# Kernel optimization log

Measured on AMD Instinct MI355X. Metric: run time of the kernel, lower is better.

Reference implementation:

```python
import jax, jax.numpy as jnp
import numpy as np

B, C, H, W = 16, 256, 56, 56
HID = C * 2            # modifier_expansion = 2
GROUPS = 8             # min(8, HID//4)
K = 3                  # inner_steps
LR = 0.01              # exp(log(inner_lr))
RATIO = 0.25           # spatial_mask_ratio
GN_EPS = 1e-5


def setup_inputs() -> dict:
    key = jax.random.key(0)
    ks = jax.random.split(key, 12)
    x = jax.random.normal(ks[0], (B, C, H, W), jnp.float32)
    # modifier params (1x1 convs stored as 2D matrices) + GroupNorm affine
    conv1_w = jax.random.normal(ks[1], (HID, C), jnp.float32) / np.sqrt(C)
    gn_gamma = 1.0 + 0.1 * jax.random.normal(ks[2], (HID,), jnp.float32)
    gn_beta = 0.1 * jax.random.normal(ks[3], (HID,), jnp.float32)
    conv2_w = jax.random.normal(ks[4], (C, HID), jnp.float32) / np.sqrt(HID)
    # surprise reconstructor (bottleneck = C//4)
    recon_w1 = jax.random.normal(ks[5], (C // 4, C), jnp.float32) / np.sqrt(C)
    recon_w2 = jax.random.normal(ks[6], (C, C // 4), jnp.float32) / np.sqrt(C // 4)
    # gate MLP
    gate_w1 = jax.random.normal(ks[7], (C // 4, C), jnp.float32) / np.sqrt(C)
    gate_b1 = jnp.zeros((C // 4,), jnp.float32)
    gate_w2 = jax.random.normal(ks[8], (1, C // 4), jnp.float32) / np.sqrt(C // 4)
    gate_b2 = jnp.zeros((1,), jnp.float32)
    residual_scale = jnp.asarray(0.05, jnp.float32)
    # EMA buffers (eval mode: frozen)
    running_mean = 0.05 * jax.random.normal(ks[9], (C,), jnp.float32)
    running_var = 1.0 + 0.05 * jax.random.uniform(ks[10], (C,), jnp.float32)
    # spatial masks: exactly int(H*W*RATIO) zeroed positions per sample, one mask
    # per inner update step (only steps 0..K-2 affect the output)
    num_mask = int(H * W * RATIO)
    rng = np.random.default_rng(0)
    r = rng.random((K - 1, B, H * W))
    idx = np.argsort(r, axis=-1)[..., :num_mask]
    m = np.ones((K - 1, B, H * W), dtype=bool)
    np.put_along_axis(m, idx, False, axis=-1)
    masks = jnp.asarray(m.reshape(K - 1, B, 1, H, W))
    return dict(x=x, conv1_w=conv1_w, gn_gamma=gn_gamma, gn_beta=gn_beta,
                conv2_w=conv2_w, recon_w1=recon_w1, recon_w2=recon_w2,
                gate_w1=gate_w1, gate_b1=gate_b1, gate_w2=gate_w2,
                gate_b2=gate_b2, residual_scale=residual_scale,
                running_mean=running_mean, running_var=running_var, masks=masks)


def _group_norm(h, gamma, beta):
    b = h.shape[0]
    hg = h.reshape(b, GROUPS, HID // GROUPS, H, W)
    mu = hg.mean(axis=(2, 3, 4), keepdims=True)
    var = hg.var(axis=(2, 3, 4), keepdims=True)  # biased, matching torch GN
    hg = (hg - mu) * jax.lax.rsqrt(var + GN_EPS)
    return hg.reshape(b, HID, H, W) * gamma[None, :, None, None] + beta[None, :, None, None]


def _modifier(feat, w1, gamma, beta, w2):
    # Conv2d 1x1 (no bias) -> GroupNorm -> GELU -> [Dropout2d: identity in eval] -> Conv2d 1x1
    h = jnp.einsum('bchw,oc->bohw', feat, w1)
    h = jax.nn.gelu(_group_norm(h, gamma, beta), approximate=False)
    return jnp.einsum('bohw,co->bchw', h, w2)


def _surprise(y, mask, rw1, rw2, rm, rv):
    mf = mask.astype(y.dtype)                       # [B,1,H,W]
    my = y * mf
    h = jax.nn.gelu(jnp.einsum('bchw,oc->bohw', my, rw1), approximate=False)
    rec = jnp.einsum('bohw,co->bchw', h, rw2)
    inv = 1.0 - mf
    recon = (((rec - y) ** 2) * inv).sum() / (inv.sum() * C + 1e-8)
    n = y.shape[0] * y.shape[2] * y.shape[3]
    cm = y.mean(axis=(0, 2, 3))                     # [C]
    cv = ((y - cm[None, :, None, None]) ** 2).sum(axis=(0, 2, 3)) / (n - 1)  # unbiased
    consist = ((cm - rm) ** 2).mean() + ((cv / (rv + 1e-8) - 1.0) ** 2).mean()
    return recon + 0.1 * consist


def reference(x, conv1_w, gn_gamma, gn_beta, conv2_w, recon_w1, recon_w2,
              gate_w1, gate_b1, gate_w2, gate_b2, residual_scale,
              running_mean, running_var, masks):
    feat = jax.lax.stop_gradient(x)  # feat_inner = features.detach()
    params = (conv1_w, gn_gamma, gn_beta, conv2_w)

    def inner_loss(p, mask):
        m = _modifier(feat, *p)
        return _surprise(m + feat, mask, recon_w1, recon_w2, running_mean, running_var)

    # TTT inner loop: K-1 SGD updates on the modifier params; updates are
    # stop_gradient'ed so the outer Jacobian wrt initial params is identity,
    # matching torch's .data in-place update with create_graph=False.
    for step in range(K - 1):
        g = jax.grad(inner_loss)(params, masks[step])
        params = tuple(p - LR * jax.lax.stop_gradient(gi) for p, gi in zip(params, g))

    modification = _modifier(x, *params)  # final forward uses non-detached features

    pooled = x.mean(axis=(2, 3))                                    # [B,C]
    gh = jax.nn.gelu(pooled @ gate_w1.T + gate_b1, approximate=False)
    gate = jax.nn.sigmoid(gh @ gate_w2.T + gate_b2)[:, :, None, None]  # [B,1,1,1]

    return x + residual_scale * gate * modification
```

## Files before the change

### kernel.cpp

```cpp
#include <hip/hip_runtime.h>
#include <math.h>


#define BB    16
#define CC    256
#define HWW   3136
#define NTOT  (BB*HWW)
#define HIDD  512
#define NGRP  8
#define GMSZ  (64*HWW)
#define C4    64
#define LRATE 0.01f
#define SKW   32
#define CHUNK (NTOT/SKW)
#define NV8   (HWW/8)
#define FSTR  132

#define EP_STORE    0
#define EP_ADDFEAT  1
#define EP_T1H      2
#define EP_DYREC    3
#define EP_DT1      4
#define EP_DYFIN    5
#define EP_H1STAT   6
// ... 90 lines not shown

__global__ void k_cvt(const void* __restrict__ src, float* __restrict__ dst, int n,
                      const int* __restrict__ dtf){
  int i = blockIdx.x*256 + threadIdx.x;
  if (i>=n) return;
  if (*dtf) dst[i] = bf2f(((const u16*)src)[i]);
  else      dst[i] = ((const float*)src)[i];
}
__global__ void k_wcvt(const float* __restrict__ src, u16* __restrict__ d,
                       u16* __restrict__ dT, int R, int Cc){
  int i = blockIdx.x*256+threadIdx.x;
  if (i >= R*Cc) return;
  int r = i/Cc, c = i - r*Cc;
  u16 v = f2bf(src[i]);
  d[i] = v;
  if (dT) dT[(size_t)c*R + r] = v;
}

__global__ void k_expand(const unsigned char* __restrict__ mraw, const int* __restrict__ flag,
                         float* __restrict__ mf, float* __restrict__ zc){
  __shared__ float sm[4];
  int i = blockIdx.x*256 + threadIdx.x;
  int f = *flag;
  float v;
  if (f==1)      v = (((const int*)mraw)[i] != 0) ? 1.f : 0.f;
  else if (f==0) v = (mraw[i] != 0) ? 1.f : 0.f;
  else if (f==2) v = (((const u16*)mraw)[i] != 0) ? 1.f : 0.f;
  else           v = (((const float*)mraw)[i] != 0.f) ? 1.f : 0.f;
  mf[i] = v;
  float S = blk_sum(1.f - v, sm);
  if (threadIdx.x==0) atomicAdd(&zc[blockIdx.x/196], S);
}

template<int MASKX,int EPI,int XDYN,int E0DYN>
__global__ __launch_bounds__(256) void k_gemm_mfma(
    const u16* __restrict__ A, const void* __restrict__ Xv, u16* __restrict__ Out,
    int K, const int* __restrict__ xdt, const float* __restrict__ mf,
    const void* __restrict__ e0, const float* __restrict__ e1,
    const float* __restrict__ e2, u16* __restrict__ o2, float* __restrict__ o3)
{
  __shared__ __align__(16) u16 Ws[64*40];
  __shared__ __align__(16) u16 Xs[128*40];
  const int t = threadIdx.x;
  const int w = t >> 6, lane = t & 63;
  const int col = lane & 15, quad = lane >> 4;
  const int M = (int)gridDim.y << 6;
  const int m0 = blockIdx.y << 6, n0 = blockIdx.x << 7;
  const int isbx = XDYN ? *xdt : 1;
  const u16*   Xb = (const u16*)Xv;
  const float* Xf = (const float*)Xv;
  const int wrow = t >> 2, wkq = (t & 3) * 8;
  const int xn   = 2*(t & 63);
  const int xq   = t >> 6;
  const int gn0  = n0 + xn;
  const int xb_  = gn0 / HWW;
  const int xs_  = gn0 - xb_*HWW;

  f32x4 acc[4][2];
  #pragma unroll
  for (int i=0;i<4;i++){
    #pragma unroll
    for (int j=0;j<2;j++) acc[i][j] = (f32x4)(0.0f);
  }

  for (int k0=0; k0<K; k0+=32){
    {
      uint4 v = *(const uint4*)(A + (size_t)(m0+wrow)*K + k0 + wkq);
      *(uint4*)(Ws + wrow*40 + wkq) = v;
    }
    {
      ushort e[16];
      size_t base = ((size_t)xb_*K + k0 + xq*8)*HWW + xs_;
      if (isbx){
        #pragma unroll
        for (int j=0;j<8;j++){
          unsigned v = *(const unsigned*)(Xb + base + (size_t)j*HWW);
          e[j]   = (ushort)(v & 0xFFFFu);
          e[8+j] = (ushort)(v >> 16);
        }
      } else {
        #pragma unroll
        for (int j=0;j<8;j++){
          float2 f = *(const float2*)(Xf + base + (size_t)j*HWW);
          e[j]   = f2bf(f.x);
          e[8+j] = f2bf(f.y);
        }
      }
      if (MASKX){
        if (mf[gn0]   == 0.f){
          #pragma unroll
          for (int j=0;j<8;j++) e[j] = 0;
        }
        if (mf[gn0+1] == 0.f){
          #pragma unroll
          for (int j=0;j<8;j++) e[8+j] = 0;
        }
      }
      *(uint4*)(Xs + xn*40     + xq*8) = pack8(e);
      *(uint4*)(Xs + (xn+1)*40 + xq*8) = pack8(e+8);
    }
    __syncthreads();
    bf16x8 af[4], bfr[2];
    #pragma unroll
    for (int mi=0;mi<4;mi++)
      af[mi] = *(const bf16x8*)(Ws + (mi*16+col)*40 + quad*8);
    #pragma unroll
    for (int nj=0;nj<2;nj++)
      bfr[nj] = *(const bf16x8*)(Xs + (w*32+nj*16+col)*40 + quad*8);
    #pragma unroll
    for (int mi=0;mi<4;mi++){
      #pragma unroll
      for (int nj=0;nj<2;nj++)
        acc[mi][nj] = __builtin_amdgcn_mfma_f32_16x16x32_bf16(af[mi], bfr[nj], acc[mi][nj], 0,0,0);
    }
    __syncthreads();
  }
  const int isb0 = E0DYN ? *xdt : 1;
  float* fst  = (float*)Xs;
  float* sred = (float*)Ws;
  const int row16 = t >> 4;
  const int cb    = (t & 15) * 8;
  const int nb8   = n0 + cb;
  const int b8    = nb8 / HWW;
  const int sb8   = nb8 - b8*HWW;
  const int bA    = n0 / HWW, bB = (n0+127)/HWW;
  const int g     = m0 >> 6;

  if (EPI==EP_H1STAT){ if (t<4) sred[t]=0.f; }
  if (EPI==EP_YADDSTAT){ for (int i=t;i<128;i+=256) sred[i]=0.f; }
  if (EPI==EP_GNB1){ for (int i=t;i<132;i+=256) sred[i]=0.f; }
  if (EPI==EP_H1STAT||EPI==EP_YADDSTAT||EPI==EP_GNB1) __syncthreads();

  float dscale=0.f, gmul=0.f, muT=0.f, rT=0.f;
  if (EPI==EP_DYREC) dscale = 2.0f / (e1[0]*(float)CC + 1e-8f);
  if (EPI==EP_OUT)   gmul = e2[0]*e1[b8];
  if (EPI==EP_GNB1){ muT = e1[b8*NGRP+g]; rT = e1[128+b8*NGRP+g]; }

  #pragma unroll
  for (int mi=0;mi<4;mi++){
    #pragma unroll
    for (int nj=0;nj<2;nj++){
      #pragma unroll
      for (int r=0;r<4;r++)
        fst[(quad*4+r)*FSTR + w*32 + nj*16 + col] = acc[mi][nj][r];
    }
    __syncthreads();
    const int m = m0 + mi*16 + row16;
    const size_t oidx = ((size_t)b8*M + m)*HWW + sb8;
    float v[8];
    {
      const float* frow = fst + row16*FSTR + cb;
      float4 p0 = *(const float4*)frow;
      float4 p1 = *(const float4*)(frow+4);
      v[0]=p0.x; v[1]=p0.y; v[2]=p0.z; v[3]=p0.w;
      v[4]=p1.x; v[5]=p1.y; v[6]=p1.z; v[7]=p1.w;
    }

    if (EPI==EP_STORE){
      *(uint4*)(Out+oidx) = pk8(v);
    }
    else if (EPI==EP_ADDFEAT){
      float xv[8];
      if (isb0) up8(*(const uint4*)((const u16*)e0+oidx), xv);
      else {
        float4 a0 = *(const float4*)((const float*)e0+oidx);
        float4 a1 = *(const float4*)((const float*)e0+oidx+4);
        xv[0]=a0.x; xv[1]=a0.y; xv[2]=a0.z; xv[3]=a0.w;
        xv[4]=a1.x; xv[5]=a1.y; xv[6]=a1.z; xv[7]=a1.w;
      }
      #pragma unroll
      for (int j=0;j<8;j++) v[j] += xv[j];
      *(uint4*)(Out+oidx) = pk8(v);
// ... 11 lines not shown
      float4 f0 = *(const float4*)(mf+nb8);
      float4 f1 = *(const float4*)(mf+nb8+4);
      mfv[0]=f0.x; mfv[1]=f0.y; mfv[2]=f0.z; mfv[3]=f0.w;
      mfv[4]=f1.x; mfv[5]=f1.y; mfv[6]=f1.z; mfv[7]=f1.w;
      #pragma unroll
      for (int j=0;j<8;j++) v[j] = (v[j]-yv[j])*(1.0f-mfv[j])*dscale;
      *(uint4*)(Out+oidx) = pk8(v);
    }
    else if (EPI==EP_DT1){
      float tv[8];
      up8(*(const uint4*)((const u16*)e0+oidx), tv);
      #pragma unroll
      for (int j=0;j<8;j++) v[j] = v[j]*gelu_g_fast(tv[j]);
      *(uint4*)(Out+oidx) = pk8(v);
    }
    else if (EPI==EP_DYFIN){
      float yv[8], dv[8], mfv[8];
      up8(*(const uint4*)((const u16*)e0+oidx), yv);
      up8(*(const uint4*)(Out+oidx), dv);
      float4 f0 = *(const float4*)(mf+nb8);
      float4 f1 = *(const float4*)(mf+nb8+4);
      mfv[0]=f0.x; mfv[1]=f0.y; mfv[2]=f0.z; mfv[3]=f0.w;
      mfv[4]=f1.x; mfv[5]=f1.y; mfv[6]=f1.z; mfv[7]=f1.w;
      const float c1 = e1[m], c2 = e2[m];
      #pragma unroll
      for (int j=0;j<8;j++) v[j] = mfv[j]*v[j] - dv[j] + c1 + c2*yv[j];
      *(uint4*)(Out+oidx) = pk8(v);
    }
    else if (EPI==EP_H1STAT){
      *(uint4*)(Out+oidx) = pk8(v);
      float s=0.f, q=0.f;
      #pragma unroll
      for (int j=0;j<8;j++){ s += v[j]; q = fmaf(v[j],v[j],q); }
      float s0 = (b8==bA)?s:0.f, q0 = (b8==bA)?q:0.f;
      float s1v = s-s0, q1v = q-q0;
      #pragma unroll
      for (int o=1;o<64;o<<=1){
        s0 += __shfl_xor(s0,o); q0 += __shfl_xor(q0,o);
        s1v += __shfl_xor(s1v,o); q1v += __shfl_xor(q1v,o);
      }
      if (lane==0){
        atomicAdd(&sred[0], s0); atomicAdd(&sred[1], q0);
        atomicAdd(&sred[2], s1v); atomicAdd(&sred[3], q1v);
      }
    }
    else if (EPI==EP_YADDSTAT){
      float xv[8];
      if (isb0) up8(*(const uint4*)((const u16*)e0+oidx), xv);
      else {
        float4 a0 = *(const float4*)((const float*)e0+oidx);
        float4 a1 = *(const float4*)((const float*)e0+oidx+4);
        xv[0]=a0.x; xv[1]=a0.y; xv[2]=a0.z; xv[3]=a0.w;
        xv[4]=a1.x; xv[5]=a1.y; xv[6]=a1.z; xv[7]=a1.w;
      }
      float s=0.f, q=0.f;
      #pragma unroll
      for (int j=0;j<8;j++){
        v[j] += xv[j];
        s += v[j]; q = fmaf(v[j],v[j],q);
      }
      *(uint4*)(Out+oidx) = pk8(v);
      #pragma unroll
      for (int o=1;o<16;o<<=1){ s += __shfl_xor(s,o); q += __shfl_xor(q,o); }
      if ((t&15)==0){
        atomicAdd(&sred[mi*16+row16], s);
        atomicAdd(&sred[64+mi*16+row16], q);
      }
    }
    else if (EPI==EP_GNB1){
      float hv[8];
      up8(*(const uint4*)((const u16*)e0+oidx), hv);
      const float go = e2[m], beo = e2[HIDD+m];
      float dB=0.f, dG=0.f, sS=0.f, sQ=0.f;
      #pragma unroll
      for (int j=0;j<8;j++){
        float hn   = (hv[j]-muT)*rT;
        float ghat = fmaf(hn, go, beo);
        float dgh  = v[j]*gelu_g_fast(ghat);
        float dhn  = dgh*go;
        v[j] = dhn;
        dB += dgh; dG = fmaf(dgh,hn,dG);
        sS += dhn; sQ = fmaf(dhn,hn,sQ);
      }
      *(uint4*)(Out+oidx) = pk8(v);
      #pragma unroll
      for (int o=1;o<16;o<<=1){ dB += __shfl_xor(dB,o); dG += __shfl_xor(dG,o); }
      if ((t&15)==0){
        atomicAdd(&sred[mi*16+row16], dB);
        atomicAdd(&sred[64+mi*16+row16], dG);
      }
      float s0 = (b8==bA)?sS:0.f, q0 = (b8==bA)?sQ:0.f;
      float s1v = sS-s0, q1v = sQ-q0;
      #pragma unroll
      for (int o=1;o<64;o<<=1){
        s0 += __shfl_xor(s0,o); q0 += __shfl_xor(q0,o);
        s1v += __shfl_xor(s1v,o); q1v += __shfl_xor(q1v,o);
      }
      if (lane==0){
        atomicAdd(&sred[128], s0); atomicAdd(&sred[129], q0);
        atomicAdd(&sred[130], s1v); atomicAdd(&sred[131], q1v);
      }
    }
    else if (EPI==EP_OUT){
      float xv[8];
      if (isb0){
        up8(*(const uint4*)((const u16*)e0+oidx), xv);
        #pragma unroll
        for (int j=0;j<8;j++) v[j] = xv[j] + gmul*v[j];
        *(uint4*)(Out+oidx) = pk8(v);
      } else {
        float4 a0 = *(const float4*)((const float*)e0+oidx);
        float4 a1 = *(const float4*)((const float*)e0+oidx+4);
        float4 r0, r1;
        r0.x = a0.x + gmul*v[0]; r0.y = a0.y + gmul*v[1];
        r0.z = a0.z + gmul*v[2]; r0.w = a0.w + gmul*v[3];
        r1.x = a1.x + gmul*v[4]; r1.y = a1.y + gmul*v[5];
        r1.z = a1.z + gmul*v[6]; r1.w = a1.w + gmul*v[7];
        *(float4*)((float*)Out+oidx)   = r0;
        *(float4*)((float*)Out+oidx+4) = r1;
      }
    }
    __syncthreads();
  }

  if (EPI==EP_H1STAT){
    if (t==0){
      atomicAdd(&o3[bA*NGRP+g],     sred[0]);
      atomicAdd(&o3[128+bA*NGRP+g], sred[1]);
    }
    if (t==1 && bB!=bA){
      atomicAdd(&o3[bB*NGRP+g],     sred[2]);
      atomicAdd(&o3[128+bB*NGRP+g], sred[3]);
    }
  }
  if (EPI==EP_YADDSTAT){
    if (t<64){
      atomicAdd(&o3[m0+t],    sred[t]);
      atomicAdd(&o3[CC+m0+t], sred[64+t]);
    }
  }
  if (EPI==EP_GNB1){
    if (t<64){
      atomicAdd(&o3[m0+t],     sred[64+t]);
      atomicAdd(&o3[512+m0+t], sred[t]);
    }
    if (t==64){
      atomicAdd(&o3[1024+bA*NGRP+g], sred[128]);
      atomicAdd(&o3[1152+bA*NGRP+g], sred[129]);
    }
    if (t==65 && bB!=bA){
      atomicAdd(&o3[1024+bB*NGRP+g], sred[130]);
      atomicAdd(&o3[1152+bB*NGRP+g], sred[131]);
    }
  }
}

template<int QDYN, int GNB2>
__global__ __launch_bounds__(256) void k_wgrad_mfma(
    const u16* __restrict__ P, const void* __restrict__ Qv, float* __restrict__ part,
    int CHP, int CHQ, const int* __restrict__ xdt, int ntx,
    const u16* __restrict__ h1, const float* __restrict__ musig,
    const float* __restrict__ red)
{
  __shared__ u16 Ps[64*40];
  __shared__ u16 Qs[64*40];
  const int f = blockIdx.x;
  const int j = f >> 3;
  const int sk = (f & 7) + ((j >> 5) << 3);
  const int tile = j & 31;
  const int ty = tile / ntx;
  const int m0 = (tile - ty*ntx) << 6;
  const int n0 = ty << 6;
  const int t = threadIdx.x;
  const int w = t >> 6, lane = t & 63;
  const int col = lane & 15, quad = lane >> 4;
  const int isbq = QDYN ? *xdt : 1;
  const u16*   Qb = (const u16*)Qv;
  const float* Qf = (const float*)Qv;
  const int srow = (t & 127) >> 1;
  const int ssq  = ((t & 127) & 1) * 16;
  f32x4 acc[2][2];
  #pragma unroll
  for (int i=0;i<2;i++){
    #pragma unroll
    for (int jj=0;jj<2;jj++) acc[i][jj] = (f32x4)(0.0f);
  }
  const int mbase = (w & 1)*32, nbase = (w >> 1)*32;

  for (int kb = sk*CHUNK; kb < sk*CHUNK + CHUNK; kb += 32){
    const int b = kb / HWW;
    const int s = kb - b*HWW;
    if (t < 128){
      size_t off = ((size_t)b*CHP + m0+srow)*HWW + s + ssq;
      uint4 v0 = *(const uint4*)(P + off);
      uint4 v1 = *(const uint4*)(P + off + 8);
      if (GNB2){
        const int bg = b*NGRP + (m0>>6);
        const float mu_ = musig[bg], r_ = musig[128+bg];
        const float a1 = red[1024+bg]*(1.0f/GMSZ);
        const float a2 = red[1152+bg]*(1.0f/GMSZ);
        uint4 h0 = *(const uint4*)(h1 + off);
        uint4 h1v = *(const uint4*)(h1 + off + 8);
        float fd[8], fh[8];
        up8(v0, fd); up8(h0, fh);
        #pragma unroll
        for (int q2=0;q2<8;q2++){ float hn=(fh[q2]-mu_)*r_; fd[q2]=r_*(fd[q2]-a1-hn*a2); }
        v0 = pk8(fd);
        up8(v1, fd); up8(h1v, fh);
        #pragma unroll
        for (int q2=0;q2<8;q2++){ float hn=(fh[q2]-mu_)*r_; fd[q2]=r_*(fd[q2]-a1-hn*a2); }
        v1 = pk8(fd);
      }
      *(uint4*)(Ps + srow*40 + ssq)     = v0;
      *(uint4*)(Ps + srow*40 + ssq + 8) = v1;
    } else {
      size_t off = ((size_t)b*CHQ + n0+srow)*HWW + s + ssq;
      if (isbq){
        uint4 v0 = *(const uint4*)(Qb + off);
        uint4 v1 = *(const uint4*)(Qb + off + 8);
        *(uint4*)(Qs + srow*40 + ssq)     = v0;
        *(uint4*)(Qs + srow*40 + ssq + 8) = v1;
      } else {
        ushort e[16];
        #pragma unroll
        for (int g2=0; g2<4; g2++){
          float4 ff = *(const float4*)(Qf + off + g2*4);
          e[g2*4+0]=f2bf(ff.x); e[g2*4+1]=f2bf(ff.y); e[g2*4+2]=f2bf(ff.z); e[g2*4+3]=f2bf(ff.w);
        }
        *(uint4*)(Qs + srow*40 + ssq)     = pack8(e);
        *(uint4*)(Qs + srow*40 + ssq + 8) = pack8(e+8);
      }
    }
    __syncthreads();
    bf16x8 pa[2], qb[2];
    #pragma unroll
    for (int a=0;a<2;a++)
      pa[a] = *(const bf16x8*)(Ps + (mbase + a*16 + col)*40 + quad*8);
    #pragma unroll
    for (int bb=0;bb<2;bb++)
      qb[bb] = *(const bf16x8*)(Qs + (nbase + bb*16 + col)*40 + quad*8);
    #pragma unroll
    for (int a=0;a<2;a++){
      #pragma unroll
      for (int bb=0;bb<2;bb++)
        acc[a][bb] = __builtin_amdgcn_mfma_f32_16x16x32_bf16(pa[a], qb[bb], acc[a][bb], 0,0,0);
    }
    __syncthreads();
  }
  float* dst = part + (size_t)sk*CHP*CHQ;
  #pragma unroll
  for (int a=0;a<2;a++){
    #pragma unroll
    for (int bb=0;bb<2;bb++){
      #pragma unroll
      for (int r=0;r<4;r++){
        const int m = m0 + mbase + a*16 + quad*4 + r;
        const int n = n0 + nbase + bb*16 + col;
        dst[(size_t)m*CHQ + n] = acc[a][bb][r];
      }
    }
  }
}
__global__ void k_wgrad_reduce(const float* __restrict__ part, float* __restrict__ dW, int n){
  int i = blockIdx.x*256+threadIdx.x;
  if (i>=n) return;
  float s=0;
  #pragma unroll
  for (int k=0;k<SKW;k++) s += part[(size_t)k*n + i];
  dW[i]=s;
}

__global__ void k_gn_finalize(const float* gsum, const float* gsumsq, float* mu, float* rsig){
  int i = threadIdx.x; if (i>=BB*NGRP) return;
// ... 204 lines not shown
  }
  u16* h1p = nullptr;
  if (off + (size_t)HIDD*NTOT*2 <= ws_size)
    h1p = (u16*)alloc((size_t)HIDD*NTOT*2);

  k_detect_dtype<<<1,1,0,stream>>>((const u16*)x_in, dtf);
  k_detect_mask<<<1,1,0,stream>>>((const unsigned char*)mk_in, mkf);
  #define CVT(src,dst,n) k_cvt<<<((n)+255)/256,256,0,stream>>>(src,dst,(n),dtf)
  CVT(w1_in,  pw1,  131072);
  CVT(g_in,   pg,   512);
  CVT(b_in,   pb,   512);
  CVT(w2_in,  pw2,  131072);
  CVT(rw1_in, rw1f, 16384);
  CVT(rw2_in, rw2f, 16384);
  CVT(gw1_in, gw1f, 16384);
  CVT(gb1_in, gb1f, 64);
  CVT(gw2_in, gw2f, 64);
  CVT(gb2_in, gb2f, 1);
  CVT(rs_in,  rsf,  1);
  CVT(rm_in,  rmf,  256);
  CVT(rv_in,  rvf,  256);
  #undef CVT
  k_wcvt<<<512,256,0,stream>>>(pw1, wb1, 0,     HIDD, CC);
  k_wcvt<<<512,256,0,stream>>>(pw2, wb2, wb2T,  CC, HIDD);
  k_wcvt<<<64,256,0,stream>>>(rw1f, rwb1, rwb1T, C4, CC);
  k_wcvt<<<64,256,0,stream>>>(rw2f, rwb2, rwb2T, CC, C4);
  hipMemsetAsync(zc, 0, 8, stream);
  k_expand<<<392,256,0,stream>>>((const unsigned char*)mk_in, mkf, mfb, zc);

  for (int s=0; s<2; s++){
    const float* mfs = mfb + s*NTOT;
    u16* h1dst = h1p ? h1p : Ab;
    hipMemsetAsync(gsum, 0, 1024, stream);
    k_gemm_mfma<0,EP_H1STAT,1,0><<<dim3(392,8),256,0,stream>>>(wb1, x_in, h1dst, CC, dtf, 0,0,0,0,0, gsum);
    k_gn_finalize<<<1,128,0,stream>>>(gsum, gsumsq, mu, rsig);
    k_gelu_fwd<1><<<BB*HIDD,256,0,stream>>>(h1dst, Ab, mu, rsig, pg, pb);
    hipMemsetAsync(cmsum, 0, 2048, stream);
    k_gemm_mfma<0,EP_YADDSTAT,0,1><<<dim3(392,4),256,0,stream>>>(wb2, Ab, ybuf, HIDD, dtf, 0, x_in, 0,0,0, cmsum);
    k_y_finalize<<<1,256,0,stream>>>(cmsum, cmsq, rmf, rvf, coefA, coefB);
    k_gemm_mfma<1,EP_T1H,0,0><<<dim3(392,1),256,0,stream>>>(rwb1, ybuf, t1b, CC, dtf, mfs, 0,0,0, hb, 0);
    k_gemm_mfma<0,EP_DYREC,0,0><<<dim3(392,4),256,0,stream>>>(rwb2, hb, dY, C4, dtf, mfs, ybuf, zc+s, 0,0, 0);
    k_gemm_mfma<0,EP_DT1,0,0><<<dim3(392,1),256,0,stream>>>(rwb2T, dY, hb, CC, dtf, 0, t1b, 0,0,0, 0);
    k_gemm_mfma<0,EP_DYFIN,0,0><<<dim3(392,4),256,0,stream>>>(rwb1T, hb, dY, C4, dtf, mfs, ybuf, coefA, coefB, 0, 0);
    k_wgrad_mfma<0,0><<<dim3(32*SKW),256,0,stream>>>(dY, Ab, part, CC, HIDD, dtf, 4, 0,0,0);
    k_wgrad_reduce<<<512,256,0,stream>>>(part, dW2, 131072);
    hipMemsetAsync(dGa, 0, 5120, stream);
    if (h1p){
      k_gemm_mfma<0,EP_GNB1,0,0><<<dim3(392,8),256,0,stream>>>(wb2T, dY, Ab, CC, dtf, 0, h1p, mu, pg, 0, dGa);
      k_wgrad_mfma<1,1><<<dim3(32*SKW),256,0,stream>>>(Ab, x_in, part, HIDD, CC, dtf, 8, h1p, mu, dGa);
    } else {
      k_gemm_mfma<0,EP_STORE,0,0><<<dim3(392,8),256,0,stream>>>(wb2T, dY, Ab, CC, dtf, 0,0,0,0,0, 0);
      k_gemm_mfma<0,EP_H1STAT,1,0><<<dim3(392,8),256,0,stream>>>(wb1, x_in, h1rc, CC, dtf, 0,0,0,0,0, gsum);
      k_gn_bwd1<<<BB*HIDD,256,0,stream>>>(Ab, h1rc, mu, rsig, pg, pb, dGa, dBe, s1, s2);
      k_gn_bwd2<<<BB*HIDD,256,0,stream>>>(Ab, h1rc, mu, rsig, s1, s2);
      k_wgrad_mfma<1,0><<<dim3(32*SKW),256,0,stream>>>(Ab, x_in, part, HIDD, CC, dtf, 8, 0,0,0);
    }
    k_wgrad_reduce<<<512,256,0,stream>>>(part, dW1, 131072);
    k_update<<<512,256,0,stream>>>(pw1, pw2, pg, pb, dW1, dW2, dGa, dBe);
    k_wcvt<<<512,256,0,stream>>>(pw1, wb1, 0,    HIDD, CC);
    k_wcvt<<<512,256,0,stream>>>(pw2, wb2, wb2T, CC, HIDD);
  }

  k_pool<<<BB*CC,256,0,stream>>>(x_in, dtf, pooled);
  k_gate<<<BB,64,0,stream>>>(pooled, gw1f, gb1f, gw2f, gb2f, gate);

  hipMemsetAsync(gsum, 0, 1024, stream);
  k_gemm_mfma<0,EP_H1STAT,1,0><<<dim3(392,8),256,0,stream>>>(wb1, x_in, Ab, CC, dtf, 0,0,0,0,0, gsum);
  k_gn_finalize<<<1,128,0,stream>>>(gsum, gsumsq, mu, rsig);
  k_gelu_fwd<0><<<BB*HIDD,256,0,stream>>>(Ab, Ab, mu, rsig, pg, pb);
  k_gemm_mfma<0,EP_OUT,0,1><<<dim3(392,4),256,0,stream>>>(wb2, Ab, (u16*)d_out, HIDD, dtf, 0, x_in, gate, rsf, 0, 0);
}
```

Measured before the change: 1.075 ms.

## Use 128-row GEMM tiles, pad LDS stride, fuse GN+GELU into output GEMM

Adds an MT template parameter so the MFMA GEMM can compute 128 output rows per block, halving grid height and reusing each loaded activation tile across more rows. LDS row stride changes from 40 to 42 to reduce bank conflicts. Per-row shared atomics in the stat epilogues become plain stores, and group statistics accumulate in registers before a single wave reduction. The final GroupNorm+GELU kernel is removed and applied on the fly while loading X into the output GEMM, with extra per-element math and more registers in exchange.

```diff
diff --git a/kernel.cpp b/kernel.cpp
--- a/kernel.cpp
+++ b/kernel.cpp
@@ -146,20 +146,23 @@
   if (threadIdx.x==0) atomicAdd(&zc[blockIdx.x/196], S);
 }
 
-template<int MASKX,int EPI,int XDYN,int E0DYN>
+template<int MASKX,int EPI,int XDYN,int E0DYN,int MT,int XGN>
 __global__ __launch_bounds__(256) void k_gemm_mfma(
     const u16* __restrict__ A, const void* __restrict__ Xv, u16* __restrict__ Out,
     int K, const int* __restrict__ xdt, const float* __restrict__ mf,
     const void* __restrict__ e0, const float* __restrict__ e1,
-    const float* __restrict__ e2, u16* __restrict__ o2, float* __restrict__ o3)
+    const float* __restrict__ e2, u16* __restrict__ o2, float* __restrict__ o3,
+    const float* __restrict__ xmu, const float* __restrict__ xpg)
 {
-  __shared__ __align__(16) u16 Ws[64*40];
-  __shared__ __align__(16) u16 Xs[128*40];
+  constexpr int MROWS = 64*MT;
+  constexpr int NMI   = 4*MT;
+  __shared__ __align__(16) u16 Ws[MROWS*42];
+  __shared__ __align__(16) u16 Xs[128*42];
   const int t = threadIdx.x;
   const int w = t >> 6, lane = t & 63;
   const int col = lane & 15, quad = lane >> 4;
-  const int M = (int)gridDim.y << 6;
-  const int m0 = blockIdx.y << 6, n0 = blockIdx.x << 7;
+  const int M = (int)gridDim.y * MROWS;
+  const int m0 = blockIdx.y * MROWS, n0 = blockIdx.x << 7;
   const int isbx = XDYN ? *xdt : 1;
   const u16*   Xb = (const u16*)Xv;
   const float* Xf = (const float*)Xv;
@@ -170,17 +173,21 @@
   const int xb_  = gn0 / HWW;
   const int xs_  = gn0 - xb_*HWW;
 
-  f32x4 acc[4][2];
+  f32x4 acc[NMI][2];
   #pragma unroll
-  for (int i=0;i<4;i++){
+  for (int i=0;i<NMI;i++){
     #pragma unroll
     for (int j=0;j<2;j++) acc[i][j] = (f32x4)(0.0f);
   }
 
   for (int k0=0; k0<K; k0+=32){
-    {
+    if (MT==2){
+      const u16* ap = A + (size_t)(m0 + (t>>1))*K + k0 + (t&1)*16;
+      *(uint4*)(Ws + (t>>1)*42 + (t&1)*16)     = *(const uint4*)ap;
+      *(uint4*)(Ws + (t>>1)*42 + (t&1)*16 + 8) = *(const uint4*)(ap+8);
+    } else {
       uint4 v = *(const uint4*)(A + (size_t)(m0+wrow)*K + k0 + wkq);
-      *(uint4*)(Ws + wrow*40 + wkq) = v;
+      *(uint4*)(Ws + wrow*42 + wkq) = v;
     }
     {
       ushort e[16];
@@ -189,8 +196,23 @@
         #pragma unroll
         for (int j=0;j<8;j++){
           unsigned v = *(const unsigned*)(Xb + base + (size_t)j*HWW);
-          e[j]   = (ushort)(v & 0xFFFFu);
-          e[8+j] = (ushort)(v >> 16);
+          if (XGN){
+            const int o  = k0 + xq*8 + j;
+            const int bg = xb_*NGRP + (o>>6);
+            const float mu_ = xmu[bg], rs_ = xmu[128+bg];
+            const float ga_ = xpg[o],  be_ = xpg[512+o];
+            float f0 = bf2f((u16)(v & 0xFFFFu));
+            float f1 = bf2f((u16)(v >> 16));
+            f0 = fmaf((f0-mu_)*rs_, ga_, be_);
+            f1 = fmaf((f1-mu_)*rs_, ga_, be_);
+            f0 = (XGN==2) ? gelu_f(f0) : gelu_fast(f0);
+            f1 = (XGN==2) ? gelu_f(f1) : gelu_fast(f1);
+            e[j]   = f2bf(f0);
+            e[8+j] = f2bf(f1);
+          } else {
+            e[j]   = (ushort)(v & 0xFFFFu);
+            e[8+j] = (ushort)(v >> 16);
+          }
         }
       } else {
         #pragma unroll
@@ -210,22 +232,19 @@
           for (int j=0;j<8;j++) e[8+j] = 0;
         }
       }
-      *(uint4*)(Xs + xn*40     + xq*8) = pack8(e);
-      *(uint4*)(Xs + (xn+1)*40 + xq*8) = pack8(e+8);
+      *(uint4*)(Xs + xn*42     + xq*8) = pack8(e);
+      *(uint4*)(Xs + (xn+1)*42 + xq*8) = pack8(e+8);
     }
     __syncthreads();
-    bf16x8 af[4], bfr[2];
-    #pragma unroll
-    for (int mi=0;mi<4;mi++)
-      af[mi] = *(const bf16x8*)(Ws + (mi*16+col)*40 + quad*8);
+    bf16x8 bfr[2];
     #pragma unroll
     for (int nj=0;nj<2;nj++)
-      bfr[nj] = *(const bf16x8*)(Xs + (w*32+nj*16+col)*40 + quad*8);
-    #pragma unroll
-    for (int mi=0;mi<4;mi++){
-      #pragma unroll
-      for (int nj=0;nj<2;nj++)
-        acc[mi][nj] = __builtin_amdgcn_mfma_f32_16x16x32_bf16(af[mi], bfr[nj], acc[mi][nj], 0,0,0);
+      bfr[nj] = *(const bf16x8*)(Xs + (w*32+nj*16+col)*42 + quad*8);
+    #pragma unroll
+    for (int mi=0;mi<NMI;mi++){
+      bf16x8 af = *(const bf16x8*)(Ws + (mi*16+col)*42 + quad*8);
+      acc[mi][0] = __builtin_amdgcn_mfma_f32_16x16x32_bf16(af, bfr[0], acc[mi][0], 0,0,0);
+      acc[mi][1] = __builtin_amdgcn_mfma_f32_16x16x32_bf16(af, bfr[1], acc[mi][1], 0,0,0);
     }
     __syncthreads();
   }
@@ -238,20 +257,21 @@
   const int b8    = nb8 / HWW;
   const int sb8   = nb8 - b8*HWW;
   const int bA    = n0 / HWW, bB = (n0+127)/HWW;
-  const int g     = m0 >> 6;
-
-  if (EPI==EP_H1STAT){ if (t<4) sred[t]=0.f; }
-  if (EPI==EP_YADDSTAT){ for (int i=t;i<128;i+=256) sred[i]=0.f; }
-  if (EPI==EP_GNB1){ for (int i=t;i<132;i+=256) sred[i]=0.f; }
-  if (EPI==EP_H1STAT||EPI==EP_YADDSTAT||EPI==EP_GNB1) __syncthreads();
-
-  float dscale=0.f, gmul=0.f, muT=0.f, rT=0.f;
+  const int gbase = m0 >> 6;
+
+  if (EPI==EP_H1STAT){ if (t < 4*MT) sred[t]=0.f; }
+  if (EPI==EP_GNB1){ if (t < 4*MT) sred[2*NMI*16 + t]=0.f; }
+  if (EPI==EP_H1STAT||EPI==EP_GNB1) __syncthreads();
+
+  float dscale=0.f, gmul=0.f;
   if (EPI==EP_DYREC) dscale = 2.0f / (e1[0]*(float)CC + 1e-8f);
   if (EPI==EP_OUT)   gmul = e2[0]*e1[b8];
-  if (EPI==EP_GNB1){ muT = e1[b8*NGRP+g]; rT = e1[128+b8*NGRP+g]; }
-
+  float hs0[MT], hq0[MT], hs1[MT], hq1[MT];
   #pragma unroll
-  for (int mi=0;mi<4;mi++){
+  for (int i=0;i<MT;i++){ hs0[i]=0.f; hq0[i]=0.f; hs1[i]=0.f; hq1[i]=0.f; }
+
+  #pragma unroll
+  for (int mi=0;mi<NMI;mi++){
     #pragma unroll
     for (int nj=0;nj<2;nj++){
       #pragma unroll
@@ -329,17 +349,9 @@
       float s=0.f, q=0.f;
       #pragma unroll
       for (int j=0;j<8;j++){ s += v[j]; q = fmaf(v[j],v[j],q); }
-      float s0 = (b8==bA)?s:0.f, q0 = (b8==bA)?q:0.f;
-      float s1v = s-s0, q1v = q-q0;
-      #pragma unroll
-      for (int o=1;o<64;o<<=1){
-        s0 += __shfl_xor(s0,o); q0 += __shfl_xor(q0,o);
-        s1v += __shfl_xor(s1v,o); q1v += __shfl_xor(q1v,o);
-      }
-      if (lane==0){
-        atomicAdd(&sred[0], s0); atomicAdd(&sred[1], q0);
-        atomicAdd(&sred[2], s1v); atomicAdd(&sred[3], q1v);
-      }
+      const bool inA = (b8==bA);
+      hs0[mi>>2] += inA ? s : 0.f;  hq0[mi>>2] += inA ? q : 0.f;
+      hs1[mi>>2] += inA ? 0.f : s;  hq1[mi>>2] += inA ? 0.f : q;
     }
     else if (EPI==EP_YADDSTAT){
       float xv[8];
@@ -360,13 +372,15 @@
       #pragma unroll
       for (int o=1;o<16;o<<=1){ s += __shfl_xor(s,o); q += __shfl_xor(q,o); }
       if ((t&15)==0){
-        atomicAdd(&sred[mi*16+row16], s);
-        atomicAdd(&sred[64+mi*16+row16], q);
+        sred[mi*16+row16]          = s;
+        sred[NMI*16 + mi*16+row16] = q;
       }
     }
     else if (EPI==EP_GNB1){
       float hv[8];
       up8(*(const uint4*)((const u16*)e0+oidx), hv);
+      const int gcur = gbase + (mi>>2);
+      const float muT = e1[b8*NGRP+gcur], rT = e1[128+b8*NGRP+gcur];
       const float go = e2[m], beo = e2[HIDD+m];
       float dB=0.f, dG=0.f, sS=0.f, sQ=0.f;
       #pragma unroll
@@ -383,20 +397,12 @@
       #pragma unroll
       for (int o=1;o<16;o<<=1){ dB += __shfl_xor(dB,o); dG += __shfl_xor(dG,o); }
       if ((t&15)==0){
-        atomicAdd(&sred[mi*16+row16], dB);
-        atomicAdd(&sred[64+mi*16+row16], dG);
-      }
-      float s0 = (b8==bA)?sS:0.f, q0 = (b8==bA)?sQ:0.f;
-      float s1v = sS-s0, q1v = sQ-q0;
-      #pragma unroll
-      for (int o=1;o<64;o<<=1){
-        s0 += __shfl_xor(s0,o); q0 += __shfl_xor(q0,o);
-        s1v += __shfl_xor(s1v,o); q1v += __shfl_xor(q1v,o);
-      }
-      if (lane==0){
-        atomicAdd(&sred[128], s0); atomicAdd(&sred[129], q0);
-        atomicAdd(&sred[130], s1v); atomicAdd(&sred[131], q1v);
-      }
+        sred[mi*16+row16]          = dB;
+        sred[NMI*16 + mi*16+row16] = dG;
+      }
+      const bool inA = (b8==bA);
+      hs0[mi>>2] += inA ? sS : 0.f;  hq0[mi>>2] += inA ? sQ : 0.f;
+      hs1[mi>>2] += inA ? 0.f : sS;  hq1[mi>>2] += inA ? 0.f : sQ;
     }
     else if (EPI==EP_OUT){
       float xv[8];
@@ -420,34 +426,66 @@
     __syncthreads();
   }
 
+  if (EPI==EP_H1STAT || EPI==EP_GNB1){
+    const int soff = (EPI==EP_GNB1) ? 2*NMI*16 : 0;
+    #pragma unroll
+    for (int g2=0; g2<MT; g2++){
+      float a0=hs0[g2], c0=hq0[g2], a1=hs1[g2], c1=hq1[g2];
+      #pragma unroll
+      for (int o=1;o<64;o<<=1){
+        a0 += __shfl_xor(a0,o); c0 += __shfl_xor(c0,o);
+        a1 += __shfl_xor(a1,o); c1 += __shfl_xor(c1,o);
+      }
+      if (lane==0){
+        atomicAdd(&sred[soff+g2*4+0], a0);
+        atomicAdd(&sred[soff+g2*4+1], c0);
+        atomicAdd(&sred[soff+g2*4+2], a1);
+        atomicAdd(&sred[soff+g2*4+3], c1);
+      }
+    }
+    __syncthreads();
+  }
+
   if (EPI==EP_H1STAT){
     if (t==0){
-      atomicAdd(&o3[bA*NGRP+g],     sred[0]);
-      atomicAdd(&o3[128+bA*NGRP+g], sred[1]);
+      #pragma unroll
+      for (int g2=0; g2<MT; g2++){
+        atomicAdd(&o3[bA*NGRP+gbase+g2],     sred[g2*4+0]);
+        atomicAdd(&o3[128+bA*NGRP+gbase+g2], sred[g2*4+1]);
+      }
     }
     if (t==1 && bB!=bA){
-      atomicAdd(&o3[bB*NGRP+g],     sred[2]);
-      atomicAdd(&o3[128+bB*NGRP+g], sred[3]);
+      #pragma unroll
+      for (int g2=0; g2<MT; g2++){
+        atomicAdd(&o3[bB*NGRP+gbase+g2],     sred[g2*4+2]);
+        atomicAdd(&o3[128+bB*NGRP+gbase+g2], sred[g2*4+3]);
+      }
     }
   }
   if (EPI==EP_YADDSTAT){
-    if (t<64){
+    if (t < NMI*16){
       atomicAdd(&o3[m0+t],    sred[t]);
-      atomicAdd(&o3[CC+m0+t], sred[64+t]);
+      atomicAdd(&o3[CC+m0+t], sred[NMI*16+t]);
     }
   }
   if (EPI==EP_GNB1){
-    if (t<64){
-      atomicAdd(&o3[m0+t],     sred[64+t]);
+    if (t < NMI*16){
+      atomicAdd(&o3[m0+t],     sred[NMI*16+t]);
       atomicAdd(&o3[512+m0+t], sred[t]);
     }
-    if (t==64){
-      atomicAdd(&o3[1024+bA*NGRP+g], sred[128]);
-      atomicAdd(&o3[1152+bA*NGRP+g], sred[129]);
-    }
-    if (t==65 && bB!=bA){
-      atomicAdd(&o3[1024+bB*NGRP+g], sred[130]);
-      atomicAdd(&o3[1152+bB*NGRP+g], sred[131]);
+    if (t==NMI*16){
+      #pragma unroll
+      for (int g2=0; g2<MT; g2++){
+        atomicAdd(&o3[1024+bA*NGRP+gbase+g2], sred[2*NMI*16+g2*4+0]);
+        atomicAdd(&o3[1152+bA*NGRP+gbase+g2], sred[2*NMI*16+g2*4+1]);
+      }
+    }
+    if (t==NMI*16+1 && bB!=bA){
+      #pragma unroll
+      for (int g2=0; g2<MT; g2++){
+        atomicAdd(&o3[1024+bB*NGRP+gbase+g2], sred[2*NMI*16+g2*4+2]);
+        atomicAdd(&o3[1152+bB*NGRP+gbase+g2], sred[2*NMI*16+g2*4+3]);
+      }
     }
   }
 }
@@ -459,8 +497,8 @@
     const u16* __restrict__ h1, const float* __restrict__ musig,
     const float* __restrict__ red)
 {
-  __shared__ u16 Ps[64*40];
-  __shared__ u16 Qs[64*40];
+  __shared__ __align__(16) u16 Ps[64*42];
+  __shared__ __align__(16) u16 Qs[64*42];
   const int f = blockIdx.x;
   const int j = f >> 3;
   const int sk = (f & 7) + ((j >> 5) << 3);
@@ -508,15 +546,15 @@
         for (int q2=0;q2<8;q2++){ float hn=(fh[q2]-mu_)*r_; fd[q2]=r_*(fd[q2]-a1-hn*a2); }
         v1 = pk8(fd);
       }
-      *(uint4*)(Ps + srow*40 + ssq)     = v0;
-      *(uint4*)(Ps + srow*40 + ssq + 8) = v1;
+      *(uint4*)(Ps + srow*42 + ssq)     = v0;
+      *(uint4*)(Ps + srow*42 + ssq + 8) = v1;
     } else {
       size_t off = ((size_t)b*CHQ + n0+srow)*HWW + s + ssq;
       if (isbq){
         uint4 v0 = *(const uint4*)(Qb + off);
         uint4 v1 = *(const uint4*)(Qb + off + 8);
-        *(uint4*)(Qs + srow*40 + ssq)     = v0;
-        *(uint4*)(Qs + srow*40 + ssq + 8) = v1;
+        *(uint4*)(Qs + srow*42 + ssq)     = v0;
+        *(uint4*)(Qs + srow*42 + ssq + 8) = v1;
       } else {
         ushort e[16];
         #pragma unroll
@@ -524,18 +562,18 @@
           float4 ff = *(const float4*)(Qf + off + g2*4);
           e[g2*4+0]=f2bf(ff.x); e[g2*4+1]=f2bf(ff.y); e[g2*4+2]=f2bf(ff.z); e[g2*4+3]=f2bf(ff.w);
         }
-        *(uint4*)(Qs + srow*40 + ssq)     = pack8(e);
-        *(uint4*)(Qs + srow*40 + ssq + 8) = pack8(e+8);
+        *(uint4*)(Qs + srow*42 + ssq)     = pack8(e);
+        *(uint4*)(Qs + srow*42 + ssq + 8) = pack8(e+8);
       }
     }
     __syncthreads();
     bf16x8 pa[2], qb[2];
     #pragma unroll
     for (int a=0;a<2;a++)
-      pa[a] = *(const bf16x8*)(Ps + (mbase + a*16 + col)*40 + quad*8);
+      pa[a] = *(const bf16x8*)(Ps + (mbase + a*16 + col)*42 + quad*8);
     #pragma unroll
     for (int bb=0;bb<2;bb++)
-      qb[bb] = *(const bf16x8*)(Qs + (nbase + bb*16 + col)*40 + quad*8);
+      qb[bb] = *(const bf16x8*)(Qs + (nbase + bb*16 + col)*42 + quad*8);
     #pragma unroll
     for (int a=0;a<2;a++){
       #pragma unroll
@@ -806,25 +844,25 @@
     const float* mfs = mfb + s*NTOT;
     u16* h1dst = h1p ? h1p : Ab;
     hipMemsetAsync(gsum, 0, 1024, stream);
-    k_gemm_mfma<0,EP_H1STAT,1,0><<<dim3(392,8),256,0,stream>>>(wb1, x_in, h1dst, CC, dtf, 0,0,0,0,0, gsum);
+    k_gemm_mfma<0,EP_H1STAT,1,0,2,0><<<dim3(392,4),256,0,stream>>>(wb1, x_in, h1dst, CC, dtf, 0,0,0,0,0, gsum, 0,0);
     k_gn_finalize<<<1,128,0,stream>>>(gsum, gsumsq, mu, rsig);
     k_gelu_fwd<1><<<BB*HIDD,256,0,stream>>>(h1dst, Ab, mu, rsig, pg, pb);
     hipMemsetAsync(cmsum, 0, 2048, stream);
-    k_gemm_mfma<0,EP_YADDSTAT,0,1><<<dim3(392,4),256,0,stream>>>(wb2, Ab, ybuf, HIDD, dtf, 0, x_in, 0,0,0, cmsum);
+    k_gemm_mfma<0,EP_YADDSTAT,0,1,2,0><<<dim3(392,2),256,0,stream>>>(wb2, Ab, ybuf, HIDD, dtf, 0, x_in, 0,0,0, cmsum, 0,0);
     k_y_finalize<<<1,256,0,stream>>>(cmsum, cmsq, rmf, rvf, coefA, coefB);
-    k_gemm_mfma<1,EP_T1H,0,0><<<dim3(392,1),256,0,stream>>>(rwb1, ybuf, t1b, CC, dtf, mfs, 0,0,0, hb, 0);
-    k_gemm_mfma<0,EP_DYREC,0,0><<<dim3(392,4),256,0,stream>>>(rwb2, hb, dY, C4, dtf, mfs, ybuf, zc+s, 0,0, 0);
-    k_gemm_mfma<0,EP_DT1,0,0><<<dim3(392,1),256,0,stream>>>(rwb2T, dY, hb, CC, dtf, 0, t1b, 0,0,0, 0);
-    k_gemm_mfma<0,EP_DYFIN,0,0><<<dim3(392,4),256,0,stream>>>(rwb1T, hb, dY, C4, dtf, mfs, ybuf, coefA, coefB, 0, 0);
+    k_gemm_mfma<1,EP_T1H,0,0,1,0><<<dim3(392,1),256,0,stream>>>(rwb1, ybuf, t1b, CC, dtf, mfs, 0,0,0, hb, 0, 0,0);
+    k_gemm_mfma<0,EP_DYREC,0,0,2,0><<<dim3(392,2),256,0,stream>>>(rwb2, hb, dY, C4, dtf, mfs, ybuf, zc+s, 0,0, 0, 0,0);
+    k_gemm_mfma<0,EP_DT1,0,0,1,0><<<dim3(392,1),256,0,stream>>>(rwb2T, dY, hb, CC, dtf, 0, t1b, 0,0,0, 0, 0,0);
+    k_gemm_mfma<0,EP_DYFIN,0,0,2,0><<<dim3(392,2),256,0,stream>>>(rwb1T, hb, dY, C4, dtf, mfs, ybuf, coefA, coefB, 0, 0, 0,0);
     k_wgrad_mfma<0,0><<<dim3(32*SKW),256,0,stream>>>(dY, Ab, part, CC, HIDD, dtf, 4, 0,0,0);
     k_wgrad_reduce<<<512,256,0,stream>>>(part, dW2, 131072);
     hipMemsetAsync(dGa, 0, 5120, stream);
     if (h1p){
-      k_gemm_mfma<0,EP_GNB1,0,0><<<dim3(392,8),256,0,stream>>>(wb2T, dY, Ab, CC, dtf, 0, h1p, mu, pg, 0, dGa);
+      k_gemm_mfma<0,EP_GNB1,0,0,2,0><<<dim3(392,4),256,0,stream>>>(wb2T, dY, Ab, CC, dtf, 0, h1p, mu, pg, 0, dGa, 0,0);
       k_wgrad_mfma<1,1><<<dim3(32*SKW),256,0,stream>>>(Ab, x_in, part, HIDD, CC, dtf, 8, h1p, mu, dGa);
     } else {
-      k_gemm_mfma<0,EP_STORE,0,0><<<dim3(392,8),256,0,stream>>>(wb2T, dY, Ab, CC, dtf, 0,0,0,0,0, 0);
-      k_gemm_mfma<0,EP_H1STAT,1,0><<<dim3(392,8),256,0,stream>>>(wb1, x_in, h1rc, CC, dtf, 0,0,0,0,0, gsum);
+      k_gemm_mfma<0,EP_STORE,0,0,2,0><<<dim3(392,4),256,0,stream>>>(wb2T, dY, Ab, CC, dtf, 0,0,0,0,0, 0, 0,0);
+      k_gemm_mfma<0,EP_H1STAT,1,0,2,0><<<dim3(392,4),256,0,stream>>>(wb1, x_in, h1rc, CC, dtf, 0,0,0,0,0, gsum, 0,0);
       k_gn_bwd1<<<BB*HIDD,256,0,stream>>>(Ab, h1rc, mu, rsig, pg, pb, dGa, dBe, s1, s2);
       k_gn_bwd2<<<BB*HIDD,256,0,stream>>>(Ab, h1rc, mu, rsig, s1, s2);
       k_wgrad_mfma<1,0><<<dim3(32*SKW),256,0,stream>>>(Ab, x_in, part, HIDD, CC, dtf, 8, 0,0,0);
@@ -839,8 +877,7 @@
   k_gate<<<BB,64,0,stream>>>(pooled, gw1f, gb1f, gw2f, gb2f, gate);
 
   hipMemsetAsync(gsum, 0, 1024, stream);
-  k_gemm_mfma<0,EP_H1STAT,1,0><<<dim3(392,8),256,0,stream>>>(wb1, x_in, Ab, CC, dtf, 0,0,0,0,0, gsum);
+  k_gemm_mfma<0,EP_H1STAT,1,0,2,0><<<dim3(392,4),256,0,stream>>>(wb1, x_in, Ab, CC, dtf, 0,0,0,0,0, gsum, 0,0);
   k_gn_finalize<<<1,128,0,stream>>>(gsum, gsumsq, mu, rsig);
-  k_gelu_fwd<0><<<BB*HIDD,256,0,stream>>>(Ab, Ab, mu, rsig, pg, pb);
-  k_gemm_mfma<0,EP_OUT,0,1><<<dim3(392,4),256,0,stream>>>(wb2, Ab, (u16*)d_out, HIDD, dtf, 0, x_in, gate, rsf, 0, 0);
-}
+  k_gemm_mfma<0,EP_OUT,0,1,2,2><<<dim3(392,2),256,0,stream>>>(wb2, Ab, (u16*)d_out, HIDD, dtf, 0, x_in, gate, rsf, 0, 0, mu, pg);
+}
```

Measured after the change: 1.173 ms. 1.09x slower.

## Fuse final GroupNorm+GELU into output GEMM operand load; pad LDS row stride

Applied to the files above, without the earlier changes.

The final forward pass no longer launches a separate GroupNorm+GELU kernel. The output GEMM now normalizes, applies the affine transform and computes exact GELU on each B-operand element as it loads it into LDS. This removes one full read and write pass over the 512-channel hidden activation. In exchange, the exact GELU is recomputed by every M-tile block (4 per column tile) along with extra per-element scalar loads. Separately, the LDS row stride in both GEMM kernels changes from 40 to 42 halfwords to alter the bank-conflict pattern.

```diff
diff --git a/kernel.cpp b/kernel.cpp
--- a/kernel.cpp
+++ b/kernel.cpp
@@ -146,15 +146,16 @@
   if (threadIdx.x==0) atomicAdd(&zc[blockIdx.x/196], S);
 }
 
-template<int MASKX,int EPI,int XDYN,int E0DYN>
+template<int MASKX,int EPI,int XDYN,int E0DYN,int XGN>
 __global__ __launch_bounds__(256) void k_gemm_mfma(
     const u16* __restrict__ A, const void* __restrict__ Xv, u16* __restrict__ Out,
     int K, const int* __restrict__ xdt, const float* __restrict__ mf,
     const void* __restrict__ e0, const float* __restrict__ e1,
-    const float* __restrict__ e2, u16* __restrict__ o2, float* __restrict__ o3)
+    const float* __restrict__ e2, u16* __restrict__ o2, float* __restrict__ o3,
+    const float* __restrict__ xmu, const float* __restrict__ xpg)
 {
-  __shared__ __align__(16) u16 Ws[64*40];
-  __shared__ __align__(16) u16 Xs[128*40];
+  __shared__ __align__(16) u16 Ws[64*42];
+  __shared__ __align__(16) u16 Xs[128*42];
   const int t = threadIdx.x;
   const int w = t >> 6, lane = t & 63;
   const int col = lane & 15, quad = lane >> 4;
@@ -180,7 +181,7 @@
   for (int k0=0; k0<K; k0+=32){
     {
       uint4 v = *(const uint4*)(A + (size_t)(m0+wrow)*K + k0 + wkq);
-      *(uint4*)(Ws + wrow*40 + wkq) = v;
+      *(uint4*)(Ws + wrow*42 + wkq) = v;
     }
     {
       ushort e[16];
@@ -189,8 +190,23 @@
         #pragma unroll
         for (int j=0;j<8;j++){
           unsigned v = *(const unsigned*)(Xb + base + (size_t)j*HWW);
-          e[j]   = (ushort)(v & 0xFFFFu);
-          e[8+j] = (ushort)(v >> 16);
+          if (XGN){
+            const int o  = k0 + xq*8 + j;
+            const int bg = xb_*NGRP + (o>>6);
+            const float mu_ = xmu[bg], rs_ = xmu[128+bg];
+            const float ga_ = xpg[o],  be_ = xpg[512+o];
+            float f0 = bf2f((u16)(v & 0xFFFFu));
+            float f1 = bf2f((u16)(v >> 16));
+            f0 = fmaf((f0-mu_)*rs_, ga_, be_);
+            f1 = fmaf((f1-mu_)*rs_, ga_, be_);
+            f0 = (XGN==2) ? gelu_f(f0) : gelu_fast(f0);
+            f1 = (XGN==2) ? gelu_f(f1) : gelu_fast(f1);
+            e[j]   = f2bf(f0);
+            e[8+j] = f2bf(f1);
+          } else {
+            e[j]   = (ushort)(v & 0xFFFFu);
+            e[8+j] = (ushort)(v >> 16);
+          }
         }
       } else {
         #pragma unroll
@@ -210,17 +226,17 @@
           for (int j=0;j<8;j++) e[8+j] = 0;
         }
       }
-      *(uint4*)(Xs + xn*40     + xq*8) = pack8(e);
-      *(uint4*)(Xs + (xn+1)*40 + xq*8) = pack8(e+8);
+      *(uint4*)(Xs + xn*42     + xq*8) = pack8(e);
+      *(uint4*)(Xs + (xn+1)*42 + xq*8) = pack8(e+8);
     }
     __syncthreads();
     bf16x8 af[4], bfr[2];
     #pragma unroll
     for (int mi=0;mi<4;mi++)
-      af[mi] = *(const bf16x8*)(Ws + (mi*16+col)*40 + quad*8);
+      af[mi] = *(const bf16x8*)(Ws + (mi*16+col)*42 + quad*8);
     #pragma unroll
     for (int nj=0;nj<2;nj++)
-      bfr[nj] = *(const bf16x8*)(Xs + (w*32+nj*16+col)*40 + quad*8);
+      bfr[nj] = *(const bf16x8*)(Xs + (w*32+nj*16+col)*42 + quad*8);
     #pragma unroll
     for (int mi=0;mi<4;mi++){
       #pragma unroll
@@ -360,7 +376,7 @@
       #pragma unroll
       for (int o=1;o<16;o<<=1){ s += __shfl_xor(s,o); q += __shfl_xor(q,o); }
       if ((t&15)==0){
-        atomicAdd(&sred[mi*16+row16], s);
+        atomicAdd(&sred[mi*16+row16],    s);
         atomicAdd(&sred[64+mi*16+row16], q);
       }
     }
@@ -383,7 +399,7 @@
       #pragma unroll
       for (int o=1;o<16;o<<=1){ dB += __shfl_xor(dB,o); dG += __shfl_xor(dG,o); }
       if ((t&15)==0){
-        atomicAdd(&sred[mi*16+row16], dB);
+        atomicAdd(&sred[mi*16+row16],    dB);
         atomicAdd(&sred[64+mi*16+row16], dG);
       }
       float s0 = (b8==bA)?sS:0.f, q0 = (b8==bA)?sQ:0.f;
@@ -459,8 +475,8 @@
     const u16* __restrict__ h1, const float* __restrict__ musig,
     const float* __restrict__ red)
 {
-  __shared__ u16 Ps[64*40];
-  __shared__ u16 Qs[64*40];
+  __shared__ __align__(16) u16 Ps[64*42];
+  __shared__ __align__(16) u16 Qs[64*42];
   const int f = blockIdx.x;
   const int j = f >> 3;
   const int sk = (f & 7) + ((j >> 5) << 3);
@@ -508,15 +524,15 @@
         for (int q2=0;q2<8;q2++){ float hn=(fh[q2]-mu_)*r_; fd[q2]=r_*(fd[q2]-a1-hn*a2); }
         v1 = pk8(fd);
       }
-      *(uint4*)(Ps + srow*40 + ssq)     = v0;
-      *(uint4*)(Ps + srow*40 + ssq + 8) = v1;
+      *(uint4*)(Ps + srow*42 + ssq)     = v0;
+      *(uint4*)(Ps + srow*42 + ssq + 8) = v1;
     } else {
       size_t off = ((size_t)b*CHQ + n0+srow)*HWW + s + ssq;
       if (isbq){
         uint4 v0 = *(const uint4*)(Qb + off);
         uint4 v1 = *(const uint4*)(Qb + off + 8);
-        *(uint4*)(Qs + srow*40 + ssq)     = v0;
-        *(uint4*)(Qs + srow*40 + ssq + 8) = v1;
+        *(uint4*)(Qs + srow*42 + ssq)     = v0;
+        *(uint4*)(Qs + srow*42 + ssq + 8) = v1;
       } else {
         ushort e[16];
         #pragma unroll
@@ -524,18 +540,18 @@
           float4 ff = *(const float4*)(Qf + off + g2*4);
           e[g2*4+0]=f2bf(ff.x); e[g2*4+1]=f2bf(ff.y); e[g2*4+2]=f2bf(ff.z); e[g2*4+3]=f2bf(ff.w);
         }
-        *(uint4*)(Qs + srow*40 + ssq)     = pack8(e);
-        *(uint4*)(Qs + srow*40 + ssq + 8) = pack8(e+8);
+        *(uint4*)(Qs + srow*42 + ssq)     = pack8(e);
+        *(uint4*)(Qs + srow*42 + ssq + 8) = pack8(e+8);
       }
     }
     __syncthreads();
     bf16x8 pa[2], qb[2];
     #pragma unroll
     for (int a=0;a<2;a++)
-      pa[a] = *(const bf16x8*)(Ps + (mbase + a*16 + col)*40 + quad*8);
+      pa[a] = *(const bf16x8*)(Ps + (mbase + a*16 + col)*42 + quad*8);
     #pragma unroll
     for (int bb=0;bb<2;bb++)
-      qb[bb] = *(const bf16x8*)(Qs + (nbase + bb*16 + col)*40 + quad*8);
+      qb[bb] = *(const bf16x8*)(Qs + (nbase + bb*16 + col)*42 + quad*8);
     #pragma unroll
     for (int a=0;a<2;a++){
       #pragma unroll
@@ -806,25 +822,25 @@
     const float* mfs = mfb + s*NTOT;
     u16* h1dst = h1p ? h1p : Ab;
     hipMemsetAsync(gsum, 0, 1024, stream);
-    k_gemm_mfma<0,EP_H1STAT,1,0><<<dim3(392,8),256,0,stream>>>(wb1, x_in, h1dst, CC, dtf, 0,0,0,0,0, gsum);
+    k_gemm_mfma<0,EP_H1STAT,1,0,0><<<dim3(392,8),256,0,stream>>>(wb1, x_in, h1dst, CC, dtf, 0,0,0,0,0, gsum, 0,0);
     k_gn_finalize<<<1,128,0,stream>>>(gsum, gsumsq, mu, rsig);
     k_gelu_fwd<1><<<BB*HIDD,256,0,stream>>>(h1dst, Ab, mu, rsig, pg, pb);
     hipMemsetAsync(cmsum, 0, 2048, stream);
-    k_gemm_mfma<0,EP_YADDSTAT,0,1><<<dim3(392,4),256,0,stream>>>(wb2, Ab, ybuf, HIDD, dtf, 0, x_in, 0,0,0, cmsum);
+    k_gemm_mfma<0,EP_YADDSTAT,0,1,0><<<dim3(392,4),256,0,stream>>>(wb2, Ab, ybuf, HIDD, dtf, 0, x_in, 0,0,0, cmsum, 0,0);
     k_y_finalize<<<1,256,0,stream>>>(cmsum, cmsq, rmf, rvf, coefA, coefB);
-    k_gemm_mfma<1,EP_T1H,0,0><<<dim3(392,1),256,0,stream>>>(rwb1, ybuf, t1b, CC, dtf, mfs, 0,0,0, hb, 0);
-    k_gemm_mfma<0,EP_DYREC,0,0><<<dim3(392,4),256,0,stream>>>(rwb2, hb, dY, C4, dtf, mfs, ybuf, zc+s, 0,0, 0);
-    k_gemm_mfma<0,EP_DT1,0,0><<<dim3(392,1),256,0,stream>>>(rwb2T, dY, hb, CC, dtf, 0, t1b, 0,0,0, 0);
-    k_gemm_mfma<0,EP_DYFIN,0,0><<<dim3(392,4),256,0,stream>>>(rwb1T, hb, dY, C4, dtf, mfs, ybuf, coefA, coefB, 0, 0);
+    k_gemm_mfma<1,EP_T1H,0,0,0><<<dim3(392,1),256,0,stream>>>(rwb1, ybuf, t1b, CC, dtf, mfs, 0,0,0, hb, 0, 0,0);
+    k_gemm_mfma<0,EP_DYREC,0,0,0><<<dim3(392,4),256,0,stream>>>(rwb2, hb, dY, C4, dtf, mfs, ybuf, zc+s, 0,0, 0, 0,0);
+    k_gemm_mfma<0,EP_DT1,0,0,0><<<dim3(392,1),256,0,stream>>>(rwb2T, dY, hb, CC, dtf, 0, t1b, 0,0,0, 0, 0,0);
+    k_gemm_mfma<0,EP_DYFIN,0,0,0><<<dim3(392,4),256,0,stream>>>(rwb1T, hb, dY, C4, dtf, mfs, ybuf, coefA, coefB, 0, 0, 0,0);
     k_wgrad_mfma<0,0><<<dim3(32*SKW),256,0,stream>>>(dY, Ab, part, CC, HIDD, dtf, 4, 0,0,0);
     k_wgrad_reduce<<<512,256,0,stream>>>(part, dW2, 131072);
     hipMemsetAsync(dGa, 0, 5120, stream);
     if (h1p){
-      k_gemm_mfma<0,EP_GNB1,0,0><<<dim3(392,8),256,0,stream>>>(wb2T, dY, Ab, CC, dtf, 0, h1p, mu, pg, 0, dGa);
+      k_gemm_mfma<0,EP_GNB1,0,0,0><<<dim3(392,8),256,0,stream>>>(wb2T, dY, Ab, CC, dtf, 0, h1p, mu, pg, 0, dGa, 0,0);
       k_wgrad_mfma<1,1><<<dim3(32*SKW),256,0,stream>>>(Ab, x_in, part, HIDD, CC, dtf, 8, h1p, mu, dGa);
     } else {
-      k_gemm_mfma<0,EP_STORE,0,0><<<dim3(392,8),256,0,stream>>>(wb2T, dY, Ab, CC, dtf, 0,0,0,0,0, 0);
-      k_gemm_mfma<0,EP_H1STAT,1,0><<<dim3(392,8),256,0,stream>>>(wb1, x_in, h1rc, CC, dtf, 0,0,0,0,0, gsum);
+      k_gemm_mfma<0,EP_STORE,0,0,0><<<dim3(392,8),256,0,stream>>>(wb2T, dY, Ab, CC, dtf, 0,0,0,0,0, 0, 0,0);
+      k_gemm_mfma<0,EP_H1STAT,1,0,0><<<dim3(392,8),256,0,stream>>>(wb1, x_in, h1rc, CC, dtf, 0,0,0,0,0, gsum, 0,0);
       k_gn_bwd1<<<BB*HIDD,256,0,stream>>>(Ab, h1rc, mu, rsig, pg, pb, dGa, dBe, s1, s2);
       k_gn_bwd2<<<BB*HIDD,256,0,stream>>>(Ab, h1rc, mu, rsig, s1, s2);
       k_wgrad_mfma<1,0><<<dim3(32*SKW),256,0,stream>>>(Ab, x_in, part, HIDD, CC, dtf, 8, 0,0,0);
@@ -839,8 +855,7 @@
   k_gate<<<BB,64,0,stream>>>(pooled, gw1f, gb1f, gw2f, gb2f, gate);
 
   hipMemsetAsync(gsum, 0, 1024, stream);
-  k_gemm_mfma<0,EP_H1STAT,1,0><<<dim3(392,8),256,0,stream>>>(wb1, x_in, Ab, CC, dtf, 0,0,0,0,0, gsum);
+  k_gemm_mfma<0,EP_H1STAT,1,0,0><<<dim3(392,8),256,0,stream>>>(wb1, x_in, Ab, CC, dtf, 0,0,0,0,0, gsum, 0,0);
   k_gn_finalize<<<1,128,0,stream>>>(gsum, gsumsq, mu, rsig);
-  k_gelu_fwd<0><<<BB*HIDD,256,0,stream>>>(Ab, Ab, mu, rsig, pg, pb);
-  k_gemm_mfma<0,EP_OUT,0,1><<<dim3(392,4),256,0,stream>>>(wb2, Ab, (u16*)d_out, HIDD, dtf, 0, x_in, gate, rsf, 0, 0);
-}
+  k_gemm_mfma<0,EP_OUT,0,1,2><<<dim3(392,4),256,0,stream>>>(wb2, Ab, (u16*)d_out, HIDD, dtf, 0, x_in, gate, rsf, 0, 0, mu, pg);
+}
```

Measured after the change: 1.192 ms. +10.9%, slower.
